# Performance work log

Measured on AMD Instinct MI355X. Metric: run time of the kernel, lower is better.

Reference implementation:

```python
import jax, jax.numpy as jnp
import numpy as np

S, B, D1, D2 = 256, 128, 1024, 1024
H1 = (D1 + D1) // 2  # 1024
H2 = (D1 + D2) // 2  # 1024


def setup_inputs() -> dict:
    key = jax.random.key(0)
    ks = jax.random.split(key, 11)
    s = lambda k, shp, fan_in: jax.random.normal(k, shp, jnp.float32) * (1.0 / np.sqrt(fan_in))
    return {
        "feature1": jax.random.normal(ks[0], (B, D1), jnp.float32),
        "feature2": jax.random.normal(ks[1], (B, D2), jnp.float32),
        "feature1_seq": jax.random.normal(ks[2], (S, B, D1), jnp.float32),
        "W11": s(ks[3], (2 * D1, H1), 2 * D1),
        "b11": jnp.zeros((H1,), jnp.float32),
        "W12": s(ks[4], (D1 + D2, H2), D1 + D2),
        "b12": jnp.zeros((H2,), jnp.float32),
        "W21": s(ks[5], (H1, 1), H1),
        "b21": jnp.zeros((1,), jnp.float32),
        "W22": s(ks[6], (H2, 1), H2),
        "b22": jnp.zeros((1,), jnp.float32),
    }


def reference(feature1, feature2, feature1_seq, W11, b11, W12, b12, W21, b21, W22, b22):
    # feature1_seq: [S, B, D1]; feature1: [B, D1]; feature2: [B, D2]
    seq_len = feature1_seq.shape[0]
    f1 = jnp.broadcast_to(feature1[None], (seq_len,) + feature1.shape)  # [S,B,D1]
    f2 = jnp.broadcast_to(feature2[None], (seq_len,) + feature2.shape)  # [S,B,D2]
    h1 = jnp.tanh(jnp.concatenate([feature1_seq, f1], axis=-1) @ W11 + b11)  # [S,B,H1]
    h2 = jnp.tanh(jnp.concatenate([feature1_seq, f2], axis=-1) @ W12 + b12)  # [S,B,H2]
    s1 = h1 @ W21 + b21  # [S,B,1]
    s2 = h2 @ W22 + b22  # [S,B,1]
    w1 = jax.nn.softmax(s1, axis=0)  # softmax over sequence dim
    w2 = jax.nn.softmax(s2, axis=0)
    # mean over sequence of (w1+w2)*seq/2 -> [B, D1]
    return jnp.mean((w1 + w2) * feature1_seq * 0.5, axis=0)
```

## Files before the change

### kernel.cpp

```cpp
#include <hip/hip_runtime.h>

#define S_LEN 256
#define B_SZ  128
#define M_ROWS (S_LEN * B_SZ)

typedef __attribute__((ext_vector_type(8))) short bf16x8;
typedef __attribute__((ext_vector_type(4))) float f32x4;

__device__ __forceinline__ unsigned short f2bf(float x) {
    unsigned u = __float_as_uint(x);
    unsigned r = (u + 0x7fffu + ((u >> 16) & 1u)) >> 16;
    return (unsigned short)r;
}

__device__ __forceinline__ void gl_lds16(const void* g, void* l) {
    __builtin_amdgcn_global_load_lds(
        (const __attribute__((address_space(1))) unsigned int*)g,
        (__attribute__((address_space(3))) unsigned int*)l,
        16, 0, 0);
}

__global__ __launch_bounds__(256) void convert_seq(const float* __restrict__ in,
                                                   unsigned short* __restrict__ out,
                                                   long n4) {
    long i = (long)blockIdx.x * blockDim.x + threadIdx.x;
    long stride = (long)gridDim.x * blockDim.x;
    for (; i < n4; i += stride) {
        float4 v = ((const float4*)in)[i];
        ushort4 o;
        o.x = f2bf(v.x); o.y = f2bf(v.y); o.z = f2bf(v.z); o.w = f2bf(v.w);
        ((ushort4*)out)[i] = o;
    }
}

__global__ __launch_bounds__(256) void convert_f(const float* __restrict__ f1,
                                                 const float* __restrict__ f2,
                                                 unsigned short* __restrict__ out) {
    int g = blockIdx.x * 256 + threadIdx.x;
    float4 v = (g < 32768) ? ((const float4*)f1)[g] : ((const float4*)f2)[g - 32768];
    ushort4 o;
    o.x = f2bf(v.x); o.y = f2bf(v.y); o.z = f2bf(v.z); o.w = f2bf(v.w);
    ((ushort4*)out)[g] = o;
}

__global__ __launch_bounds__(256) void transpose_w(const float* __restrict__ W11,
                                                   const float* __restrict__ W12,
                                                   unsigned short* __restrict__ Wt) {
    const int nt = blockIdx.x, kt = blockIdx.y, layer = blockIdx.z;
    const float* W = layer ? W12 : W11;
    __shared__ float T[64][65];
    const int c = threadIdx.x & 63, r4 = threadIdx.x >> 6;
    const int k0 = kt * 64, n0 = nt * 64;
    #pragma unroll
    for (int p = 0; p < 16; ++p) {
        int r = p * 4 + r4;
        T[r][c] = W[(size_t)(k0 + r) * 1024 + n0 + c];
    }
    __syncthreads();
    unsigned short* Wl = Wt + (size_t)layer * 1024 * 2048;
    #pragma unroll
    for (int p = 0; p < 16; ++p) {
        int n = p * 4 + r4;
        Wl[(size_t)(n0 + n) * 2048 + k0 + c] = f2bf(T[c][n]);
    }
}

__global__ __launch_bounds__(256) void c_precompute(const unsigned short* __restrict__ fbf,
                                                    const unsigned short* __restrict__ Wt,
                                                    const float* __restrict__ b11,
                                                    const float* __restrict__ b12,
                                                    float* __restrict__ cbuf) {
    __shared__ char smem[32768];
    unsigned short* ldsA = (unsigned short*)smem;
    unsigned short* ldsB = (unsigned short*)(smem + 16384);
    const int n0 = blockIdx.x * 128;
    const int layer = blockIdx.y;
    const int tid = threadIdx.x;
    const int w = tid >> 6, l = tid & 63;
    const int wm = w >> 1, wn = w & 1;
    const int lr = l & 15, lg = l >> 4;
    const unsigned short* Af = fbf + (size_t)layer * 128 * 1024;
    const unsigned short* Wl = Wt + (size_t)layer * 1024 * 2048;
    const float* bias = layer ? b12 : b11;

    f32x4 acc[4][4];
    #pragma unroll
    for (int i = 0; i < 4; ++i)
        #pragma unroll
        for (int j = 0; j < 4; ++j)
            #pragma unroll
            for (int e = 0; e < 4; ++e) acc[i][j][e] = 0.f;

    for (int kk = 0; kk < 1024; kk += 64) {
        __syncthreads();
        #pragma unroll
        for (int c = 0; c < 4; ++c) {
            int o = w * 4096 + c * 1024;
            int ob = o + l * 16;
            int row = ob >> 7, kb = ob & 127;
            gl_lds16((const char*)Af + ((size_t)row * 1024 + kk) * 2 + kb, (char*)ldsA + o);
            gl_lds16((const char*)Wl + ((size_t)(n0 + row) * 2048 + 1024 + kk) * 2 + kb, (char*)ldsB + o);
        }
        __syncthreads();
        #pragma unroll
        for (int ks = 0; ks < 2; ++ks) {
            bf16x8 av[4], bv[4];
            #pragma unroll
            for (int i = 0; i < 4; ++i) {
                av[i] = *(const bf16x8*)(ldsA + (wm * 64 + i * 16 + lr) * 64 + ks * 32 + lg * 8);
                bv[i] = *(const bf16x8*)(ldsB + (wn * 64 + i * 16 + lr) * 64 + ks * 32 + lg * 8);
            }
            #pragma unroll
            for (int i = 0; i < 4; ++i)
                #pragma unroll
                for (int j = 0; j < 4; ++j)
                    acc[i][j] = __builtin_amdgcn_mfma_f32_16x16x32_bf16(av[i], bv[j], acc[i][j], 0, 0, 0);
        }
    }
    float* cl = cbuf + (size_t)layer * 128 * 1024;
    #pragma unroll
    for (int i = 0; i < 4; ++i)
        #pragma unroll
        for (int j = 0; j < 4; ++j)
            #pragma unroll
            for (int q = 0; q < 4; ++q) {
                int rr = wm * 64 + i * 16 + lg * 4 + q;
                int hc = n0 + wn * 64 + j * 16 + lr;
                cl[(size_t)rr * 1024 + hc] = acc[i][j][q] + bias[hc];
            }
}


__global__ __launch_bounds__(512, 2) void fused_main(const unsigned short* __restrict__ Abf,
                                                     const unsigned short* __restrict__ Wt,
                                                     const float* __restrict__ cbuf,
                                                     const float* __restrict__ W21,
                                                     const float* __restrict__ W22,
                                                     float* __restrict__ sbufp) {
    __shared__ char smem[98304];
    const int bid = blockIdx.x;
    const int r8  = bid & 7;
    const int jj  = bid >> 3;
    const int mt  = r8 + 8 * (jj & 15);
    const int g   = jj >> 4;
    const int layer = g >> 2;
    const int nt    = g & 3;
    const int n0 = nt * 256;

    const int tid = threadIdx.x;
    const int w = tid >> 6, l = tid & 63;
    const int wm = w >> 2, wn = w & 3;
    const int lr = l & 15, lg = l >> 4;

    const char* Ag = (const char*)Abf + (size_t)mt * 256 * 2048;
    const char* Bg = (const char*)(Wt + (size_t)layer * 1024 * 2048) + (size_t)n0 * 4096;

    const int dl0 = w * 1024 + l * 16;
    const int dl1 = 8192 + dl0;
    const int g0 = dl0 ^ (((dl0 >> 7) & 3) << 4);
    const int g1 = dl1 ^ (((dl1 >> 7) & 3) << 4);
    const char* srcA0 = Ag + (size_t)(g0 >> 6) * 2048 + (g0 & 63);
    const char* srcA1 = Ag + (size_t)(g1 >> 6) * 2048 + (g1 & 63);
    const char* srcB0 = Bg + (size_t)(g0 >> 6) * 4096 + (g0 & 63);
    const char* srcB1 = Bg + (size_t)(g1 >> 6) * 4096 + (g1 & 63);
    const int dstA0 = w * 1024, dstA1 = 8192 + w * 1024;

    f32x4 acc[8][4];
    #pragma unroll
    for (int i = 0; i < 8; ++i)
        #pragma unroll
        for (int j = 0; j < 4; ++j)
            #pragma unroll
            for (int e = 0; e < 4; ++e) acc[i][j][e] = 0.f;

    int offA[8], offB[4];
    #pragma unroll
    for (int i = 0; i < 8; ++i) {
        int oa = (wm * 128 + i * 16 + lr) * 64 + lg * 16;
        offA[i] = oa ^ (((oa >> 7) & 3) << 4);
    }
    #pragma unroll
    for (int j = 0; j < 4; ++j) {
        int ob = (wn * 64 + j * 16 + lr) * 64 + lg * 16;
        offB[j] = ob ^ (((ob >> 7) & 3) << 4);
    }

#define STAGE(t, bi) do {                                              \
        char* ab_ = smem + (bi) * 32768;                               \
        gl_lds16(srcA0 + (size_t)(t) * 64, ab_ + dstA0);               \
        gl_lds16(srcA1 + (size_t)(t) * 64, ab_ + dstA1);               \
        gl_lds16(srcB0 + (size_t)(t) * 64, ab_ + 16384 + dstA0);       \
        gl_lds16(srcB1 + (size_t)(t) * 64, ab_ + 16384 + dstA1);       \
    } while (0)

#define COMPUTE(bi) do {                                               \
        const char* Ab_ = smem + (bi) * 32768;                         \
        const char* Bb_ = Ab_ + 16384;                                 \
        bf16x8 av_[8], bv_[4];                                         \
        _Pragma("unroll")                                              \
        for (int i_ = 0; i_ < 8; ++i_) av_[i_] = *(const bf16x8*)(Ab_ + offA[i_]); \
        _Pragma("unroll")                                              \
        for (int j_ = 0; j_ < 4; ++j_) bv_[j_] = *(const bf16x8*)(Bb_ + offB[j_]); \
        _Pragma("unroll")                                              \
        for (int i_ = 0; i_ < 8; ++i_)                                 \
            _Pragma("unroll")                                          \
            for (int j_ = 0; j_ < 4; ++j_)                             \
                acc[i_][j_] = __builtin_amdgcn_mfma_f32_16x16x32_bf16( \
                    av_[i_], bv_[j_], acc[i_][j_], 0, 0, 0);           \
    } while (0)

#define PIPEBAR() do {                                                 \
        __builtin_amdgcn_sched_barrier(0);                             \
        asm volatile("s_waitcnt vmcnt(4)" ::: "memory");               \
        __builtin_amdgcn_sched_barrier(0);                             \
        __builtin_amdgcn_s_barrier();                                  \
        __builtin_amdgcn_sched_barrier(0);                             \
    } while (0)

    STAGE(0, 0);
    STAGE(1, 1);
    PIPEBAR();

    for (int tt = 0; tt < 30; tt += 3) {
        STAGE(tt + 2, 2); COMPUTE(0); PIPEBAR();
        STAGE(tt + 3, 0); COMPUTE(1); PIPEBAR();
        STAGE(tt + 4, 1); COMPUTE(2); PIPEBAR();
    }
    COMPUTE(0);
    __builtin_amdgcn_sched_barrier(0);
    asm volatile("s_waitcnt vmcnt(0)" ::: "memory");
    __builtin_amdgcn_sched_barrier(0);
    __builtin_amdgcn_s_barrier();
    __builtin_amdgcn_sched_barrier(0);
    COMPUTE(1);

#undef STAGE
#undef COMPUTE
#undef PIPEBAR

    __syncthreads();

    const float* cl = cbuf + (size_t)layer * 131072;
    const float* W2 = layer ? W22 : W21;
    float w2v[4];
    #pragma unroll
    for (int j = 0; j < 4; ++j) w2v[j] = W2[n0 + wn * 64 + j * 16 + lr];
    float* red = (float*)smem;
    #pragma unroll
    for (int i = 0; i < 8; ++i) {
        #pragma unroll
        for (int q = 0; q < 4; ++q) {
            int wrow = wm * 128 + i * 16 + lg * 4 + q;
            int brow = wrow & 127;
            float p = 0.f;
            #pragma unroll
            for (int j = 0; j < 4; ++j) {
                int col = n0 + wn * 64 + j * 16 + lr;
                float z = acc[i][j][q] + cl[(size_t)brow * 1024 + col];
                float e = __expf(2.f * z);
                p += (1.f - 2.f / (e + 1.f)) * w2v[j];
            }
            p += __shfl_xor(p, 1);
            p += __shfl_xor(p, 2);
            p += __shfl_xor(p, 4);
            p += __shfl_xor(p, 8);
            if (lr == 0) red[wrow * 4 + wn] = p;
        }
    }
    __syncthreads();
    if (tid < 256) {
        float v = red[tid * 4 + 0] + red[tid * 4 + 1] + red[tid * 4 + 2] + red[tid * 4 + 3];
        sbufp[(size_t)g * M_ROWS + (size_t)mt * 256 + tid] = v;
    }
}

__device__ __forceinline__ float block_max(float v, float* lds) {
    #pragma unroll
    for (int m = 32; m; m >>= 1) v = fmaxf(v, __shfl_xor(v, m));
    if ((threadIdx.x & 63) == 0) lds[threadIdx.x >> 6] = v;
    __syncthreads();
    v = fmaxf(fmaxf(lds[0], lds[1]), fmaxf(lds[2], lds[3]));
    __syncthreads();
    return v;
}
__device__ __forceinline__ float block_sum(float v, float* lds) {
    #pragma unroll
    for (int m = 32; m; m >>= 1) v += __shfl_xor(v, m);
    if ((threadIdx.x & 63) == 0) lds[threadIdx.x >> 6] = v;
    __syncthreads();
    v = lds[0] + lds[1] + lds[2] + lds[3];
    __syncthreads();
    return v;
}

__global__ __launch_bounds__(256) void coef_kernel(const float* __restrict__ sbufp,
                                                   float* __restrict__ coef,
                                                   float* __restrict__ out) {
    __shared__ float lds[4];
    const int b = blockIdx.x, s = threadIdx.x;
    float v1 = 0.f, v2 = 0.f;
    #pragma unroll
    for (int nt = 0; nt < 4; ++nt) {
        v1 += sbufp[(size_t)nt * M_ROWS + (size_t)s * 128 + b];
        v2 += sbufp[(size_t)(4 + nt) * M_ROWS + (size_t)s * 128 + b];
    }
    float m1 = block_max(v1, lds);
    float e1 = expf(v1 - m1);
    float S1 = block_sum(e1, lds);
    float m2 = block_max(v2, lds);
    float e2 = expf(v2 - m2);
    float S2 = block_sum(e2, lds);
    coef[(size_t)s * 128 + b] = (e1 / S1 + e2 / S2) * (0.5f / (float)S_LEN);
    float4 z4; z4.x = z4.y = z4.z = z4.w = 0.f;
    ((float4*)out)[(size_t)b * 256 + s] = z4;
}

__global__ __launch_bounds__(256) void final_kernel(const float* __restrict__ seq,
                                                    const float* __restrict__ coef,
                                                    float* __restrict__ out) {
    const int b = blockIdx.x, q = blockIdx.y;
    const int d0 = threadIdx.x * 4;
    float4 a; a.x = a.y = a.z = a.w = 0.f;
    for (int si = 0; si < 32; ++si) {
        int s = q * 32 + si;
        float cf = coef[(size_t)s * 128 + b];
        float4 v = *(const float4*)(seq + ((size_t)(s * 128 + b) * 1024 + d0));
        a.x += cf * v.x; a.y += cf * v.y; a.z += cf * v.z; a.w += cf * v.w;
    }
    float* o = out + (size_t)b * 1024 + d0;
    atomicAdd(o + 0, a.x);
    atomicAdd(o + 1, a.y);
    atomicAdd(o + 2, a.z);
    atomicAdd(o + 3, a.w);
}

extern "C" void kernel_launch(void* const* d_in, const int* in_sizes, int n_in,
                              void* d_out, int out_size, void* d_ws, size_t ws_size,
                              hipStream_t stream) {
    const float* feature1 = (const float*)d_in[0];
    const float* feature2 = (const float*)d_in[1];
    const float* seq      = (const float*)d_in[2];
    const float* W11      = (const float*)d_in[3];
    const float* b11      = (const float*)d_in[4];
    const float* W12      = (const float*)d_in[5];
    const float* b12      = (const float*)d_in[6];
    const float* W21      = (const float*)d_in[7];
    const float* W22      = (const float*)d_in[9];
    float* out = (float*)d_out;

    char* ws = (char*)d_ws;
    unsigned short* Abf   = (unsigned short*)(ws + 0);
    unsigned short* Wt    = (unsigned short*)(ws + 67108864);
    unsigned short* fbf   = (unsigned short*)(ws + 75497472);
    float*          cbuf  = (float*)(ws + 76021760);
    float*          sbufp = (float*)(ws + 77070336);
    float*          coef  = (float*)(ws + 78118912);

    convert_seq<<<2048, 256, 0, stream>>>(seq, Abf, (long)M_ROWS * 1024 / 4);
    convert_f<<<256, 256, 0, stream>>>(feature1, feature2, fbf);
    transpose_w<<<dim3(16, 32, 2), 256, 0, stream>>>(W11, W12, Wt);
    c_precompute<<<dim3(8, 2), 256, 0, stream>>>(fbf, Wt, b11, b12, cbuf);
    fused_main<<<1024, 512, 0, stream>>>(Abf, Wt, cbuf, W21, W22, sbufp);
    coef_kernel<<<128, 256, 0, stream>>>(sbufp, coef, out);
    final_kernel<<<dim3(128, 8), 256, 0, stream>>>(seq, coef, out);
}
```

Measured before the change: 276.2 us.

## Use 16-wave blocks with a four-stage LDS pipeline in fused GEMM

```diff
diff --git a/kernel.cpp b/kernel.cpp
--- a/kernel.cpp
+++ b/kernel.cpp
@@ -131,13 +131,13 @@
 }
 
 
-__global__ __launch_bounds__(512, 2) void fused_main(const unsigned short* __restrict__ Abf,
-                                                     const unsigned short* __restrict__ Wt,
-                                                     const float* __restrict__ cbuf,
-                                                     const float* __restrict__ W21,
-                                                     const float* __restrict__ W22,
-                                                     float* __restrict__ sbufp) {
-    __shared__ char smem[98304];
+__global__ __launch_bounds__(1024, 4) void fused_main(const unsigned short* __restrict__ Abf,
+                                                      const unsigned short* __restrict__ Wt,
+                                                      const float* __restrict__ cbuf,
+                                                      const float* __restrict__ W21,
+                                                      const float* __restrict__ W22,
+                                                      float* __restrict__ sbufp) {
+    __shared__ char smem[131072];
     const int bid = blockIdx.x;
     const int r8  = bid & 7;
     const int jj  = bid >> 3;
@@ -155,63 +155,54 @@
     const char* Ag = (const char*)Abf + (size_t)mt * 256 * 2048;
     const char* Bg = (const char*)(Wt + (size_t)layer * 1024 * 2048) + (size_t)n0 * 4096;
 
-    const int dl0 = w * 1024 + l * 16;
-    const int dl1 = 8192 + dl0;
-    const int g0 = dl0 ^ (((dl0 >> 7) & 3) << 4);
-    const int g1 = dl1 ^ (((dl1 >> 7) & 3) << 4);
-    const char* srcA0 = Ag + (size_t)(g0 >> 6) * 2048 + (g0 & 63);
-    const char* srcA1 = Ag + (size_t)(g1 >> 6) * 2048 + (g1 & 63);
-    const char* srcB0 = Bg + (size_t)(g0 >> 6) * 4096 + (g0 & 63);
-    const char* srcB1 = Bg + (size_t)(g1 >> 6) * 4096 + (g1 & 63);
-    const int dstA0 = w * 1024, dstA1 = 8192 + w * 1024;
-
-    f32x4 acc[8][4];
-    #pragma unroll
-    for (int i = 0; i < 8; ++i)
+    const int dloc = w * 1024 + l * 16;
+    const int gsw  = dloc ^ (((dloc >> 7) & 3) << 4);
+    const char* srcA = Ag + (size_t)(gsw >> 6) * 2048 + (gsw & 63);
+    const char* srcB = Bg + (size_t)(gsw >> 6) * 4096 + (gsw & 63);
+    const int dstA = w * 1024;
+
+    f32x4 acc[4][4];
+    #pragma unroll
+    for (int i = 0; i < 4; ++i)
         #pragma unroll
         for (int j = 0; j < 4; ++j)
             #pragma unroll
             for (int e = 0; e < 4; ++e) acc[i][j][e] = 0.f;
 
-    int offA[8], offB[4];
-    #pragma unroll
-    for (int i = 0; i < 8; ++i) {
-        int oa = (wm * 128 + i * 16 + lr) * 64 + lg * 16;
+    int offA[4], offB[4];
+    #pragma unroll
+    for (int i = 0; i < 4; ++i) {
+        int oa = (wm * 64 + i * 16 + lr) * 64 + lg * 16;
         offA[i] = oa ^ (((oa >> 7) & 3) << 4);
-    }
-    #pragma unroll
-    for (int j = 0; j < 4; ++j) {
-        int ob = (wn * 64 + j * 16 + lr) * 64 + lg * 16;
-        offB[j] = ob ^ (((ob >> 7) & 3) << 4);
+        int ob = (wn * 64 + i * 16 + lr) * 64 + lg * 16;
+        offB[i] = ob ^ (((ob >> 7) & 3) << 4);
     }
 
 #define STAGE(t, bi) do {                                              \
         char* ab_ = smem + (bi) * 32768;                               \
-        gl_lds16(srcA0 + (size_t)(t) * 64, ab_ + dstA0);               \
-        gl_lds16(srcA1 + (size_t)(t) * 64, ab_ + dstA1);               \
-        gl_lds16(srcB0 + (size_t)(t) * 64, ab_ + 16384 + dstA0);       \
-        gl_lds16(srcB1 + (size_t)(t) * 64, ab_ + 16384 + dstA1);       \
+        gl_lds16(srcA + (size_t)(t) * 64, ab_ + dstA);                 \
+        gl_lds16(srcB + (size_t)(t) * 64, ab_ + 16384 + dstA);         \
     } while (0)
 
 #define COMPUTE(bi) do {                                               \
         const char* Ab_ = smem + (bi) * 32768;                         \
         const char* Bb_ = Ab_ + 16384;                                 \
-        bf16x8 av_[8], bv_[4];                                         \
+        bf16x8 av_[4], bv_[4];                                         \
         _Pragma("unroll")                                              \
-        for (int i_ = 0; i_ < 8; ++i_) av_[i_] = *(const bf16x8*)(Ab_ + offA[i_]); \
+        for (int i_ = 0; i_ < 4; ++i_) av_[i_] = *(const bf16x8*)(Ab_ + offA[i_]); \
         _Pragma("unroll")                                              \
         for (int j_ = 0; j_ < 4; ++j_) bv_[j_] = *(const bf16x8*)(Bb_ + offB[j_]); \
         _Pragma("unroll")                                              \
-        for (int i_ = 0; i_ < 8; ++i_)                                 \
+        for (int i_ = 0; i_ < 4; ++i_)                                 \
             _Pragma("unroll")                                          \
             for (int j_ = 0; j_ < 4; ++j_)                             \
                 acc[i_][j_] = __builtin_amdgcn_mfma_f32_16x16x32_bf16( \
                     av_[i_], bv_[j_], acc[i_][j_], 0, 0, 0);           \
     } while (0)
 
-#define PIPEBAR() do {                                                 \
+#define WAITBAR(n) do {                                                \
         __builtin_amdgcn_sched_barrier(0);                             \
-        asm volatile("s_waitcnt vmcnt(4)" ::: "memory");               \
+        asm volatile("s_waitcnt vmcnt(" #n ")" ::: "memory");          \
         __builtin_amdgcn_sched_barrier(0);                             \
         __builtin_amdgcn_s_barrier();                                  \
         __builtin_amdgcn_sched_barrier(0);                             \
@@ -219,24 +210,22 @@
 
     STAGE(0, 0);
     STAGE(1, 1);
-    PIPEBAR();
-
-    for (int tt = 0; tt < 30; tt += 3) {
-        STAGE(tt + 2, 2); COMPUTE(0); PIPEBAR();
-        STAGE(tt + 3, 0); COMPUTE(1); PIPEBAR();
-        STAGE(tt + 4, 1); COMPUTE(2); PIPEBAR();
-    }
-    COMPUTE(0);
-    __builtin_amdgcn_sched_barrier(0);
-    asm volatile("s_waitcnt vmcnt(0)" ::: "memory");
-    __builtin_amdgcn_sched_barrier(0);
-    __builtin_amdgcn_s_barrier();
-    __builtin_amdgcn_sched_barrier(0);
-    COMPUTE(1);
+    STAGE(2, 2);
+
+    for (int tt = 0; tt < 28; tt += 4) {
+        WAITBAR(4); COMPUTE(0); STAGE(tt + 3, 3);
+        WAITBAR(4); COMPUTE(1); STAGE(tt + 4, 0);
+        WAITBAR(4); COMPUTE(2); STAGE(tt + 5, 1);
+        WAITBAR(4); COMPUTE(3); STAGE(tt + 6, 2);
+    }
+    WAITBAR(4); COMPUTE(0); STAGE(31, 3);
+    WAITBAR(4); COMPUTE(1);
+    WAITBAR(2); COMPUTE(2);
+    WAITBAR(0); COMPUTE(3);
 
 #undef STAGE
 #undef COMPUTE
-#undef PIPEBAR
+#undef WAITBAR
 
     __syncthreads();
 
@@ -247,10 +236,10 @@
     for (int j = 0; j < 4; ++j) w2v[j] = W2[n0 + wn * 64 + j * 16 + lr];
     float* red = (float*)smem;
     #pragma unroll
-    for (int i = 0; i < 8; ++i) {
+    for (int i = 0; i < 4; ++i) {
         #pragma unroll
         for (int q = 0; q < 4; ++q) {
-            int wrow = wm * 128 + i * 16 + lg * 4 + q;
+            int wrow = wm * 64 + i * 16 + lg * 4 + q;
             int brow = wrow & 127;
             float p = 0.f;
             #pragma unroll
@@ -360,7 +349,7 @@
     convert_f<<<256, 256, 0, stream>>>(feature1, feature2, fbf);
     transpose_w<<<dim3(16, 32, 2), 256, 0, stream>>>(W11, W12, Wt);
     c_precompute<<<dim3(8, 2), 256, 0, stream>>>(fbf, Wt, b11, b12, cbuf);
-    fused_main<<<1024, 512, 0, stream>>>(Abf, Wt, cbuf, W21, W22, sbufp);
+    fused_main<<<1024, 1024, 0, stream>>>(Abf, Wt, cbuf, W21, W22, sbufp);
     coef_kernel<<<128, 256, 0, stream>>>(sbufp, coef, out);
     final_kernel<<<dim3(128, 8), 256, 0, stream>>>(seq, coef, out);
 }
```

Result: faster. 256.7 us (-7.1%).

## Restructure GEMM mainloop with 64-wide K tiles and register-prefetched fragments

Applied to the files above, without the earlier changes.

```diff
diff --git a/kernel.cpp b/kernel.cpp
--- a/kernel.cpp
+++ b/kernel.cpp
@@ -137,12 +137,13 @@
                                                      const float* __restrict__ W21,
                                                      const float* __restrict__ W22,
                                                      float* __restrict__ sbufp) {
-    __shared__ char smem[98304];
+    __shared__ char smem[131072];
     const int bid = blockIdx.x;
-    const int r8  = bid & 7;
-    const int jj  = bid >> 3;
-    const int mt  = r8 + 8 * (jj & 15);
-    const int g   = jj >> 4;
+    const int xcd = bid & 7;
+    const int idx = bid >> 3;
+    const int mtq = (idx & 3) + 4 * (idx >> 5);
+    const int g   = (idx >> 2) & 7;
+    const int mt  = xcd + 8 * mtq;
     const int layer = g >> 2;
     const int nt    = g & 3;
     const int n0 = nt * 256;
@@ -155,15 +156,18 @@
     const char* Ag = (const char*)Abf + (size_t)mt * 256 * 2048;
     const char* Bg = (const char*)(Wt + (size_t)layer * 1024 * 2048) + (size_t)n0 * 4096;
 
-    const int dl0 = w * 1024 + l * 16;
-    const int dl1 = 8192 + dl0;
-    const int g0 = dl0 ^ (((dl0 >> 7) & 3) << 4);
-    const int g1 = dl1 ^ (((dl1 >> 7) & 3) << 4);
-    const char* srcA0 = Ag + (size_t)(g0 >> 6) * 2048 + (g0 & 63);
-    const char* srcA1 = Ag + (size_t)(g1 >> 6) * 2048 + (g1 & 63);
-    const char* srcB0 = Bg + (size_t)(g0 >> 6) * 4096 + (g0 & 63);
-    const char* srcB1 = Bg + (size_t)(g1 >> 6) * 4096 + (g1 & 63);
-    const int dstA0 = w * 1024, dstA1 = 8192 + w * 1024;
+    const int dloc = tid * 16;
+    const int gsw  = dloc ^ ((dloc >> 3) & 0x70);
+    const int rowS = gsw >> 7, colS = gsw & 127;
+    const char* srcA = Ag + (size_t)rowS * 2048 + colS;
+    const char* srcB = Bg + (size_t)rowS * 4096 + colS;
+    const int dstT = w * 1024;
+
+    const int xr = (lr & 7) << 4;
+    const int colx0 = (lg * 16) ^ xr;
+    const int colx1 = (lg * 16 + 64) ^ xr;
+    const int baseA = (wm * 128 + lr) * 128;
+    const int baseB = 32768 + (wn * 64 + lr) * 128;
 
     f32x4 acc[8][4];
     #pragma unroll
@@ -173,70 +177,65 @@
             #pragma unroll
             for (int e = 0; e < 4; ++e) acc[i][j][e] = 0.f;
 
-    int offA[8], offB[4];
-    #pragma unroll
-    for (int i = 0; i < 8; ++i) {
-        int oa = (wm * 128 + i * 16 + lr) * 64 + lg * 16;
-        offA[i] = oa ^ (((oa >> 7) & 3) << 4);
-    }
-    #pragma unroll
-    for (int j = 0; j < 4; ++j) {
-        int ob = (wn * 64 + j * 16 + lr) * 64 + lg * 16;
-        offB[j] = ob ^ (((ob >> 7) & 3) << 4);
-    }
-
-#define STAGE(t, bi) do {                                              \
-        char* ab_ = smem + (bi) * 32768;                               \
-        gl_lds16(srcA0 + (size_t)(t) * 64, ab_ + dstA0);               \
-        gl_lds16(srcA1 + (size_t)(t) * 64, ab_ + dstA1);               \
-        gl_lds16(srcB0 + (size_t)(t) * 64, ab_ + 16384 + dstA0);       \
-        gl_lds16(srcB1 + (size_t)(t) * 64, ab_ + 16384 + dstA1);       \
+    bf16x8 fA0[8], fA1[8], fB0[4], fB1[4];
+
+#define STAGE(t) do {                                                   \
+        char* d_ = smem + ((t) & 1) * 65536;                            \
+        const char* a_ = srcA + (size_t)(t) * 128;                      \
+        const char* b_ = srcB + (size_t)(t) * 128;                      \
+        _Pragma("unroll")                                               \
+        for (int r_ = 0; r_ < 4; ++r_) {                                \
+            gl_lds16(a_ + r_ * 131072, d_ + r_ * 8192 + dstT);          \
+            gl_lds16(b_ + r_ * 262144, d_ + 32768 + r_ * 8192 + dstT);  \
+        }                                                               \
     } while (0)
 
-#define COMPUTE(bi) do {                                               \
-        const char* Ab_ = smem + (bi) * 32768;                         \
-        const char* Bb_ = Ab_ + 16384;                                 \
-        bf16x8 av_[8], bv_[4];                                         \
-        _Pragma("unroll")                                              \
-        for (int i_ = 0; i_ < 8; ++i_) av_[i_] = *(const bf16x8*)(Ab_ + offA[i_]); \
-        _Pragma("unroll")                                              \
-        for (int j_ = 0; j_ < 4; ++j_) bv_[j_] = *(const bf16x8*)(Bb_ + offB[j_]); \
-        _Pragma("unroll")                                              \
-        for (int i_ = 0; i_ < 8; ++i_)                                 \
-            _Pragma("unroll")                                          \
-            for (int j_ = 0; j_ < 4; ++j_)                             \
-                acc[i_][j_] = __builtin_amdgcn_mfma_f32_16x16x32_bf16( \
-                    av_[i_], bv_[j_], acc[i_][j_], 0, 0, 0);           \
+#define LOADF(sA, sB, bo, cx) do {                                      \
+        const char* ba_ = smem + (bo) + baseA;                          \
+        const char* bb_ = smem + (bo) + baseB;                          \
+        _Pragma("unroll")                                               \
+        for (int i_ = 0; i_ < 8; ++i_) sA[i_] = *(const bf16x8*)(ba_ + i_ * 2048 + (cx)); \
+        _Pragma("unroll")                                               \
+        for (int j_ = 0; j_ < 4; ++j_) sB[j_] = *(const bf16x8*)(bb_ + j_ * 2048 + (cx)); \
     } while (0)
 
-#define PIPEBAR() do {                                                 \
-        __builtin_amdgcn_sched_barrier(0);                             \
-        asm volatile("s_waitcnt vmcnt(4)" ::: "memory");               \
-        __builtin_amdgcn_sched_barrier(0);                             \
-        __builtin_amdgcn_s_barrier();                                  \
-        __builtin_amdgcn_sched_barrier(0);                             \
+#define MF(sA, sB) do {                                                 \
+        _Pragma("unroll")                                               \
+        for (int i_ = 0; i_ < 8; ++i_)                                  \
+            _Pragma("unroll")                                           \
+            for (int j_ = 0; j_ < 4; ++j_)                              \
+                acc[i_][j_] = __builtin_amdgcn_mfma_f32_16x16x32_bf16(  \
+                    sA[i_], sB[j_], acc[i_][j_], 0, 0, 0);              \
     } while (0)
 
-    STAGE(0, 0);
-    STAGE(1, 1);
-    PIPEBAR();
-
-    for (int tt = 0; tt < 30; tt += 3) {
-        STAGE(tt + 2, 2); COMPUTE(0); PIPEBAR();
-        STAGE(tt + 3, 0); COMPUTE(1); PIPEBAR();
-        STAGE(tt + 4, 1); COMPUTE(2); PIPEBAR();
-    }
-    COMPUTE(0);
+    STAGE(0);
+    STAGE(1);
     __builtin_amdgcn_sched_barrier(0);
-    asm volatile("s_waitcnt vmcnt(0)" ::: "memory");
+    asm volatile("s_waitcnt vmcnt(8)" ::: "memory");
     __builtin_amdgcn_sched_barrier(0);
     __builtin_amdgcn_s_barrier();
     __builtin_amdgcn_sched_barrier(0);
-    COMPUTE(1);
+    LOADF(fA0, fB0, 0, colx0);
+
+    for (int t = 0; t < 16; ++t) {
+        const int bo = (t & 1) * 65536;
+        LOADF(fA1, fB1, bo, colx1);
+        MF(fA0, fB0);
+        __builtin_amdgcn_sched_barrier(0);
+        asm volatile("s_waitcnt lgkmcnt(0)" ::: "memory");
+        asm volatile("s_waitcnt vmcnt(0)" ::: "memory");
+        __builtin_amdgcn_sched_barrier(0);
+        __builtin_amdgcn_s_barrier();
+        __builtin_amdgcn_sched_barrier(0);
+        if (t < 14) STAGE(t + 2);
+        if (t < 15) LOADF(fA0, fB0, bo ^ 65536, colx0);
+        MF(fA1, fB1);
+        __builtin_amdgcn_sched_barrier(0);
+    }
 
 #undef STAGE
-#undef COMPUTE
-#undef PIPEBAR
+#undef LOADF
+#undef MF
 
     __syncthreads();
 
```

After: 262.0 us. -5.1%, faster.
